# Performance work log

Measured on AMD Instinct MI355X. Metric: run time of the kernel, lower is better.

Reference implementation:

```python
import jax, jax.numpy as jnp
import numpy as np

B, S, D = 1024, 200, 128
NQ, NC, NQD, NCD = 50000, 1000, 101, 101


def _linear_params(k, fan_in, fan_out):
    bound = 1.0 / np.sqrt(fan_in)
    kw, kb = jax.random.split(k)
    W = jax.random.uniform(kw, (fan_out, fan_in), minval=-bound, maxval=bound, dtype=jnp.float32)
    b = jax.random.uniform(kb, (fan_out,), minval=-bound, maxval=bound, dtype=jnp.float32)
    return W, b


def setup_inputs() -> dict:
    key = jax.random.key(0)
    ks = jax.random.split(key, 17)
    Wx, bx = _linear_params(ks[0], 4 * D, D)
    Ws1, bs1 = _linear_params(ks[1], D, D)
    Ws2, bs2 = _linear_params(ks[2], D, D)
    Wp1, bp1 = _linear_params(ks[3], 2 * D, D)
    Wp2, bp2 = _linear_params(ks[4], 2 * D, D)
    Wk, bk = _linear_params(ks[5], 4 * D, D)
    Eq = jax.random.normal(ks[6], (NQ, D), dtype=jnp.float32)
    Ec = jax.random.normal(ks[7], (NC, D), dtype=jnp.float32)
    Eqd = jax.random.normal(ks[8], (NQD, D), dtype=jnp.float32)
    Ecd = jax.random.normal(ks[9], (NCD, D), dtype=jnp.float32)
    Ecorr = jax.random.normal(ks[10], (2, D), dtype=jnp.float32)
    # xavier_uniform init for h_pre (torch: gain*sqrt(6/(fan_in+fan_out)) on [B,D])
    bh = np.sqrt(6.0 / (B + D))
    h0 = jax.random.uniform(ks[11], (B, D), minval=-bh, maxval=bh, dtype=jnp.float32)
    question_seq = jax.random.randint(ks[12], (B, S), 0, NQ)
    concept_seq = jax.random.randint(ks[13], (B, S), 0, NC)
    question_diff_seq = jax.random.randint(ks[14], (B, S), 0, NQD)
    concept_diff_seq = jax.random.randint(ks[15], (B, S), 0, NCD)
    correct_seq = jax.random.randint(ks[16], (B, S), 0, 2)
    return dict(question_seq=question_seq, concept_seq=concept_seq,
                question_diff_seq=question_diff_seq, concept_diff_seq=concept_diff_seq,
                correct_seq=correct_seq,
                Eq=Eq, Ec=Ec, Eqd=Eqd, Ecd=Ecd, Ecorr=Ecorr,
                Wx=Wx, bx=bx, Ws1=Ws1, bs1=bs1, Ws2=Ws2, bs2=bs2,
                Wp1=Wp1, bp1=bp1, Wp2=Wp2, bp2=bp2, Wk=Wk, bk=bk, h0=h0)


def reference(question_seq, concept_seq, question_diff_seq, concept_diff_seq, correct_seq,
              Eq, Ec, Eqd, Ecd, Ecorr,
              Wx, bx, Ws1, bs1, Ws2, bs2, Wp1, bp1, Wp2, bp2, Wk, bk, h0):
    qe = Eq[question_seq]            # [B,S,D]
    ce = Ec[concept_seq]
    qde = Eqd[question_diff_seq]
    cde = Ecd[concept_diff_seq]
    corr = Ecorr[correct_seq]
    # generate_x_MLP applied to all timesteps at once (same math as per-step)
    x = jnp.concatenate([qe, ce, qde, cde], axis=-1) @ Wx.T + bx  # [B,S,D]
    # time-major inputs for the scan over t = 0 .. S-2
    xs = (jnp.swapaxes(x[:, :-1], 0, 1),      # x_t       [S-1,B,D]
          jnp.swapaxes(x[:, 1:], 0, 1),       # x_{t+1}
          jnp.swapaxes(corr[:, :-1], 0, 1),
          jnp.swapaxes(qde[:, :-1], 0, 1),
          jnp.swapaxes(cde[:, :-1], 0, 1))

    def step(h_pre, inp):
        xt, xnext, ct, qdt, cdt = inp
        s_in = xt - h_pre
        sdf = jax.nn.sigmoid(s_in @ Ws1.T + bs1) * jnp.tanh(s_in @ Ws2.T + bs2)  # dropout=eval identity
        p_in = jnp.concatenate([sdf, ct], axis=-1)
        pka = jax.nn.sigmoid(p_in @ Wp1.T + bp1) * jnp.tanh(p_in @ Wp2.T + bp2)
        k_in = jnp.concatenate([h_pre, ct, qdt, cdt], axis=-1)
        g = jax.nn.sigmoid(k_in @ Wk.T + bk)
        h = g * h_pre + (1.0 - g) * pka
        yt = jax.nn.sigmoid(jnp.sum(xnext * h, axis=-1))  # [B]
        return h, yt

    _, ys = jax.lax.scan(step, h0, xs)  # ys: [S-1,B]
    y = jnp.concatenate([ys.T, jnp.zeros((question_seq.shape[0], 1), x.dtype)], axis=1)  # [B,S], y[:, S-1]=0
    return y
```

## Files before the change

kernel.cpp:

```cpp
#include <hip/hip_runtime.h>
#include <hip/hip_bf16.h>


#define S_LEN 200
#define NBATCH 1024
#define DIM 128
#define LOG2E 1.4426950408889634f

typedef short short8 __attribute__((ext_vector_type(8)));
typedef float f32x4 __attribute__((ext_vector_type(4)));

__device__ __forceinline__ unsigned short f2b(float f) {
  union { float f; unsigned u; } v; v.f = f;
  unsigned r = (v.u + 0x7FFFu + ((v.u >> 16) & 1u)) >> 16;
  return (unsigned short)r;
}
__device__ __forceinline__ float b2f(unsigned short b) {
  union { unsigned u; float f; } v; v.u = ((unsigned)b) << 16;
  return v.f;
}
__device__ __forceinline__ unsigned pk_bf16(float lo, float hi) {
  __hip_bfloat162 t = __float22bfloat162_rn(make_float2(lo, hi));
  union { __hip_bfloat162 h; unsigned u; } cv; cv.h = t;
  return cv.u;
}
__device__ __forceinline__ float sigtanh(float a, float b) {
  a = fminf(a, 30.0f);
  b = fminf(b, 15.0f);
  const float u = __builtin_amdgcn_exp2f(LOG2E * a);
  const float v = __builtin_amdgcn_exp2f(2.0f * LOG2E * b);
  return (u * (v - 1.0f)) * __builtin_amdgcn_rcpf((1.0f + u) * (v + 1.0f));
}
__device__ __forceinline__ float fast_sigmoid(float x) {
  x = fmaxf(x, -30.0f);
  return __builtin_amdgcn_rcpf(1.0f + __builtin_amdgcn_exp2f(-LOG2E * x));
}
__device__ __forceinline__ void wg_barrier_lds() {
  __asm__ volatile("s_waitcnt lgkmcnt(0)\n\ts_barrier" ::: "memory");
}

__global__ void proj_all_kernel(const float* __restrict__ Eq, const float* __restrict__ Ec,
                                const float* __restrict__ Eqd, const float* __restrict__ Ecd,
                                const float* __restrict__ Ecorr,
                                const float* __restrict__ Wx,
                                const float* __restrict__ Wp1, const float* __restrict__ bp1,
                                const float* __restrict__ Wp2, const float* __restrict__ bp2,
                                const float* __restrict__ Wk, const float* __restrict__ bk,
                                unsigned short* __restrict__ Tq, unsigned short* __restrict__ Tc,
                                unsigned short* __restrict__ Tqd, unsigned short* __restrict__ Tcd,
                                unsigned short* __restrict__ Tkqd, unsigned short* __restrict__ Tkcd,
                                float* __restrict__ Tkc, float* __restrict__ Tp1c,
                                float* __restrict__ Tp2c) {
  const int bid = blockIdx.x;
  const int tid = threadIdx.x;
  if (bid >= 802) {
    const int blk = bid - 802;
    if (blk < 101) {
      const int o = tid & 127, half = tid >> 7;
      const float* e = (half ? Ecd : Eqd) + (size_t)blk * DIM;
      const float* wr = Wk + (size_t)o * 512 + (half ? 384 : 256);
      float a = 0.f;
      for (int k = 0; k < DIM; ++k) a = fmaf(e[k], wr[k], a);
      (half ? Tkcd : Tkqd)[blk * DIM + o] = f2b(a);
    } else {
      for (int idx = tid; idx < 768; idx += 256) {
        const int t = idx >> 8, e = (idx >> 7) & 1, o = idx & 127;
        const float* ec = Ecorr + e * DIM;
        const float* wr; float bias; float* dst;
        if (t == 0)      { wr = Wp1 + (size_t)o * 256 + 128; bias = bp1[o]; dst = Tp1c; }
        else if (t == 1) { wr = Wp2 + (size_t)o * 256 + 128; bias = bp2[o]; dst = Tp2c; }
        else             { wr = Wk  + (size_t)o * 512 + 128; bias = bk[o];  dst = Tkc;  }
        float a = bias;
        for (int k = 0; k < DIM; ++k) a = fmaf(ec[k], wr[k], a);
        dst[e * DIM + o] = a;
      }
    }
    return;
  }
  const float* E; int M, coff, r0; unsigned short* T;
  if (bid < 782)      { E = Eq;  M = 50000; coff = 0;   T = Tq;  r0 = bid * 64; }
  else if (bid < 798) { E = Ec;  M = 1000;  coff = 128; T = Tc;  r0 = (bid - 782) * 64; }
  else if (bid < 800) { E = Eqd; M = 101;   coff = 256; T = Tqd; r0 = (bid - 798) * 64; }
  else                { E = Ecd; M = 101;   coff = 384; T = Tcd; r0 = (bid - 800) * 64; }

  __shared__ __align__(16) unsigned short A[64][136];
  {
    const int row = tid >> 2, cb = (tid & 3) * 32;
    union U8 { uint4 v; unsigned short s[8]; } o;
#pragma unroll
    for (int cc = 0; cc < 4; ++cc) {
      const int c8 = cb + cc * 8;
      if (r0 + row < M) {
        const float4 e0 = *(const float4*)(E + (size_t)(r0 + row) * DIM + c8);
        const float4 e1 = *(const float4*)(E + (size_t)(r0 + row) * DIM + c8 + 4);
        o.s[0] = f2b(e0.x); o.s[1] = f2b(e0.y); o.s[2] = f2b(e0.z); o.s[3] = f2b(e0.w);
        o.s[4] = f2b(e1.x); o.s[5] = f2b(e1.y); o.s[6] = f2b(e1.z); o.s[7] = f2b(e1.w);
      } else {
        o.v = make_uint4(0, 0, 0, 0);
      }
      *(uint4*)&A[row][c8] = o.v;
    }
  }
  __syncthreads();
  const int w = tid >> 6, L = tid & 63, q = L >> 4, m = L & 15;
  short8 bf[2][4];
#pragma unroll
  for (int T2 = 0; T2 < 2; ++T2) {
    const int n = 32 * w + 16 * T2 + m;
#pragma unroll
    for (int kb = 0; kb < 4; ++kb) {
      const float* src = Wx + (size_t)n * 512 + coff + kb * 32 + q * 8;
      const float4 v0 = *(const float4*)src;
      const float4 v1 = *(const float4*)(src + 4);
      short8 f;
      f[0] = (short)f2b(v0.x); f[1] = (short)f2b(v0.y);
      f[2] = (short)f2b(v0.z); f[3] = (short)f2b(v0.w);
      f[4] = (short)f2b(v1.x); f[5] = (short)f2b(v1.y);
      f[6] = (short)f2b(v1.z); f[7] = (short)f2b(v1.w);
      bf[T2][kb] = f;
    }
  }
  const f32x4 vzero = {0.f, 0.f, 0.f, 0.f};
#pragma unroll
  for (int mt = 0; mt < 4; ++mt) {
    short8 af[4];
#pragma unroll
    for (int kb = 0; kb < 4; ++kb) af[kb] = *(const short8*)&A[mt * 16 + m][kb * 32 + q * 8];
    f32x4 acc[2] = {vzero, vzero};
#pragma unroll
    for (int kb = 0; kb < 4; ++kb) {
#pragma unroll
      for (int T2 = 0; T2 < 2; ++T2)
        acc[T2] = __builtin_amdgcn_mfma_f32_16x16x32_bf16(af[kb], bf[T2][kb], acc[T2], 0, 0, 0);
    }
#pragma unroll
    for (int T2 = 0; T2 < 2; ++T2) {
      const int col = 32 * w + 16 * T2 + m;
#pragma unroll
      for (int i = 0; i < 4; ++i) {
        const int r = r0 + mt * 16 + q * 4 + i;
        if (r < M) T[(size_t)r * DIM + col] = f2b(acc[T2][i]);
      }
    }
  }
}

__global__ void build_x_kernel(const int* __restrict__ qs, const int* __restrict__ cs,
                               const int* __restrict__ qds, const int* __restrict__ cds,
                               const int* __restrict__ corr,
                               const unsigned short* __restrict__ Tq, const unsigned short* __restrict__ Tc,
                               const unsigned short* __restrict__ Tqd, const unsigned short* __restrict__ Tcd,
                               const float* __restrict__ bx, unsigned short* __restrict__ xg,
                               float* __restrict__ corrf) {
  const int r0 = blockIdx.x * 32;
  const int c8 = (threadIdx.x & 15) * 8;
  const float4 bx0 = *(const float4*)(bx + c8);
  const float4 bx1 = *(const float4*)(bx + c8 + 4);
  float bb[8] = {bx0.x, bx0.y, bx0.z, bx0.w, bx1.x, bx1.y, bx1.z, bx1.w};
  union U8 { uint4 v; unsigned short s[8]; };
#pragma unroll
  for (int half = 0; half < 2; ++half) {
    const int r = r0 + (threadIdx.x >> 4) + half * 16;
    const int s = r >> 10, b = r & 1023;
    const int q = qs[b * S_LEN + s], c = cs[b * S_LEN + s];
    const int qd = qds[b * S_LEN + s], cd = cds[b * S_LEN + s];
    U8 vq, vc, vd, ve, o;
    vq.v = *(const uint4*)(Tq + (size_t)q * DIM + c8);
    vc.v = *(const uint4*)(Tc + (size_t)c * DIM + c8);
    vd.v = *(const uint4*)(Tqd + (size_t)qd * DIM + c8);
    ve.v = *(const uint4*)(Tcd + (size_t)cd * DIM + c8);
#pragma unroll
    for (int j = 0; j < 8; ++j)
      o.s[j] = f2b(b2f(vq.s[j]) + b2f(vc.s[j]) + b2f(vd.s[j]) + b2f(ve.s[j]) + bb[j]);
    *(uint4*)(xg + (size_t)r * DIM + c8) = o.v;
    if ((threadIdx.x & 15) == 0) corrf[r] = (float)corr[b * S_LEN + s];
  }
}

__global__ void gemm_xg_kernel(const unsigned short* __restrict__ xg,
                               const float* __restrict__ Wk,
                               const int* __restrict__ corr, const int* __restrict__ qds,
                               const int* __restrict__ cds,
                               const float* __restrict__ Tkc,
                               const unsigned short* __restrict__ Tkqd,
                               const unsigned short* __restrict__ Tkcd,
                               unsigned short* __restrict__ GG) {
  const int tid = threadIdx.x;
  const int r0 = blockIdx.x * 128;
  __shared__ __align__(16) unsigned short TS[128][136];
#pragma unroll
  for (int it = 0; it < 2; ++it) {
    const int idx = tid + 256 * it;
    const int row = idx >> 2, cb = (idx & 3) * 32;
    const int r = r0 + row, t = r >> 10, b = r & 1023;
    const int ci = corr[b * S_LEN + t], qi = qds[b * S_LEN + t], di = cds[b * S_LEN + t];
    union U8 { uint4 v; unsigned short s[8]; };
#pragma unroll
    for (int cc = 0; cc < 4; ++cc) {
      const int c8 = cb + cc * 8;
      U8 vq, vc, o;
      vq.v = *(const uint4*)(Tkqd + (size_t)qi * DIM + c8);
      vc.v = *(const uint4*)(Tkcd + (size_t)di * DIM + c8);
      const float4 k0 = *(const float4*)(Tkc + (size_t)ci * DIM + c8);
      const float4 k1 = *(const float4*)(Tkc + (size_t)ci * DIM + c8 + 4);
      float kk[8] = {k0.x, k0.y, k0.z, k0.w, k1.x, k1.y, k1.z, k1.w};
#pragma unroll
      for (int j = 0; j < 8; ++j) o.s[j] = f2b(kk[j] + b2f(vq.s[j]) + b2f(vc.s[j]));
      *(uint4*)&TS[row][c8] = o.v;
    }
  }
  __syncthreads();
  const int w = tid >> 6, L = tid & 63, q = L >> 4, m = L & 15;
  short8 wk[2][4];
#pragma unroll
  for (int T = 0; T < 2; ++T) {
    const int n = 32 * w + 16 * T + m;
#pragma unroll
    for (int kb = 0; kb < 4; ++kb) {
      const float* src = Wk + (size_t)n * 512 + kb * 32 + q * 8;
      const float4 v0 = *(const float4*)src;
      const float4 v1 = *(const float4*)(src + 4);
      short8 f;
      f[0] = (short)f2b(v0.x); f[1] = (short)f2b(v0.y);
      f[2] = (short)f2b(v0.z); f[3] = (short)f2b(v0.w);
      f[4] = (short)f2b(v1.x); f[5] = (short)f2b(v1.y);
      f[6] = (short)f2b(v1.z); f[7] = (short)f2b(v1.w);
      wk[T][kb] = f;
    }
  }
  const f32x4 vzero = {0.f, 0.f, 0.f, 0.f};
#pragma unroll
  for (int mt = 0; mt < 8; ++mt) {
    short8 af[4];
#pragma unroll
    for (int kb = 0; kb < 4; ++kb)
      af[kb] = *(const short8*)(xg + (size_t)(r0 + mt * 16 + m) * DIM + kb * 32 + q * 8);
    f32x4 acc[2] = {vzero, vzero};
#pragma unroll
    for (int kb = 0; kb < 4; ++kb) {
#pragma unroll
      for (int T = 0; T < 2; ++T)
        acc[T] = __builtin_amdgcn_mfma_f32_16x16x32_bf16(af[kb], wk[T][kb], acc[T], 0, 0, 0);
    }
#pragma unroll
    for (int T = 0; T < 2; ++T) {
      const int col = 32 * w + 16 * T + m;
#pragma unroll
      for (int i = 0; i < 4; ++i) {
        const int row128 = mt * 16 + q * 4 + i;
        GG[(size_t)(r0 + row128) * DIM + col] = f2b(acc[T][i] + b2f(TS[row128][col]));
      }
    }
  }
}

__global__ __launch_bounds__(512, 2) void scan_kernel(
    const unsigned short* __restrict__ xg,
    const unsigned short* __restrict__ gg,
    const float* __restrict__ corrf,
    const float* __restrict__ h0,
    const float* __restrict__ Ws1, const float* __restrict__ bs1,
    const float* __restrict__ Ws2, const float* __restrict__ bs2,
    const float* __restrict__ Wp1, const float* __restrict__ Wp2,
    const float* __restrict__ Wk,
    const float* __restrict__ gTp1c, const float* __restrict__ gTp2c,
    float* __restrict__ outp) {
  __shared__ __align__(16) unsigned short Sbuf[16][136];
  __shared__ __align__(16) unsigned short Pbuf[16][136];
  __shared__ float DotBuf[16][9];

  const int tid = threadIdx.x;
  const int w = tid >> 6, L = tid & 63, q = L >> 4, m = L & 15;
  const int col16 = 16 * w + m;
  const int rbase = blockIdx.x << 4;
  const size_t SB = (size_t)NBATCH * DIM;

  short8 wf[5][4];
  {
    const float* Wptr[5] = {Ws1, Ws2, Wp1, Wp2, Wk};
    const int ldw[5] = {128, 128, 256, 256, 512};
#pragma unroll
    for (int M = 0; M < 5; ++M) {
#pragma unroll
      for (int kb = 0; kb < 4; ++kb) {
        const float* src = Wptr[M] + (size_t)col16 * ldw[M] + kb * 32 + q * 8;
        const float4 v0 = *(const float4*)src;
        const float4 v1 = *(const float4*)(src + 4);
        short8 f;
        f[0] = (short)f2b(v0.x); f[1] = (short)f2b(v0.y);
        f[2] = (short)f2b(v0.z); f[3] = (short)f2b(v0.w);
        f[4] = (short)f2b(v1.x); f[5] = (short)f2b(v1.y);
        f[6] = (short)f2b(v1.z); f[7] = (short)f2b(v1.w);
        wf[M][kb] = f;
      }
    }
  }
  const float bs1v = bs1[col16], bs2v = bs2[col16];
  const float tp1v0 = gTp1c[col16], dtp1 = gTp1c[DIM + col16] - tp1v0;
  const float tp2v0 = gTp2c[col16], dtp2 = gTp2c[DIM + col16] - tp2v0;

  float h[4];
#pragma unroll
  for (int i = 0; i < 4; ++i) {
    const int b = rbase + q * 4 + i;
    const float hv = h0[(size_t)b * DIM + col16];
    h[i] = hv;
    const float xt = b2f(xg[(size_t)b * DIM + col16]);
    Sbuf[q * 4 + i][col16] = f2b(xt - hv);
  }
  if (tid < 16) outp[(size_t)(rbase + tid) * S_LEN + (S_LEN - 1)] = 0.0f;

  unsigned short XPA[4], XPB[4], GPA[4], GPB[4];
  float4 CFA, CFB;
  const unsigned short* pxA = xg + 3 * SB + (size_t)(rbase + q * 4) * DIM + col16;
  const unsigned short* pxB = pxA + SB;
  const unsigned short* pgA = gg + 2 * SB + (size_t)(rbase + q * 4) * DIM + col16;
  const unsigned short* pgB = pgA + SB;
  const float* pcA = corrf + 2 * NBATCH + rbase + q * 4;
  const float* pcB = pcA + NBATCH;
#pragma unroll
  for (int i = 0; i < 4; ++i) {
    XPA[i] = xg[SB + (size_t)(rbase + q * 4 + i) * DIM + col16];
    XPB[i] = xg[2 * SB + (size_t)(rbase + q * 4 + i) * DIM + col16];
    GPA[i] = gg[(size_t)(rbase + q * 4 + i) * DIM + col16];
    GPB[i] = gg[SB + (size_t)(rbase + q * 4 + i) * DIM + col16];
  }
  CFA = *(const float4*)(corrf + rbase + q * 4);
  CFB = *(const float4*)(corrf + NBATCH + rbase + q * 4);

  float dotp[4] = {0.f, 0.f, 0.f, 0.f};
  const f32x4 vzero = {0.f, 0.f, 0.f, 0.f};

#define STEP(TCUR, XP, GP, CF, PX, PG, PC)                                     \
  do {                                                                         \
    const int t_ = (TCUR);                                                     \
    wg_barrier_lds();                  \
      \
    short8 sf[4];                                                              \
    _Pragma("unroll") for (int kb = 0; kb < 4; ++kb)                           \
        sf[kb] = *(const short8*)&Sbuf[m][kb * 32 + q * 8];                    \
    float xnv[4], ggv[4], cfv[4];                                              \
    _Pragma("unroll") for (int i = 0; i < 4; ++i) {                            \
      xnv[i] = b2f(XP[i]); ggv[i] = b2f(GP[i]);                                \
    }                                                                          \
    cfv[0] = CF.x; cfv[1] = CF.y; cfv[2] = CF.z; cfv[3] = CF.w;                \
    _Pragma("unroll") for (int i = 0; i < 4; ++i) {                            \
      XP[i] = PX[i * DIM]; GP[i] = PG[i * DIM];                                \
    }                                                                          \
    CF = *(const float4*)PC;                                                   \
    PX += 2 * SB; PG += 2 * SB; PC += 2 * NBATCH;                              \
    {                  \
      float dr0 = dotp[0], dr1 = dotp[1], dr2 = dotp[2], dr3 = dotp[3];        \
      _Pragma("unroll") for (int off = 1; off <= 8; off <<= 1) {               \
        dr0 += __shfl_xor(dr0, off, 64);                                       \
        dr1 += __shfl_xor(dr1, off, 64);                                       \
        dr2 += __shfl_xor(dr2, off, 64);                                       \
        dr3 += __shfl_xor(dr3, off, 64);                                       \
      }                                                                        \
      if (m == 0) {                                                            \
        DotBuf[q * 4 + 0][w] = dr0;                                            \
        DotBuf[q * 4 + 1][w] = dr1;                                            \
        DotBuf[q * 4 + 2][w] = dr2;                                            \
        DotBuf[q * 4 + 3][w] = dr3;                                            \
      }                                                                        \
    }                                                                          \
    f32x4 a1 = vzero, a2 = vzero, c1 = vzero;                                  \
    _Pragma("unroll") for (int kb = 0; kb < 4; ++kb) {                         \
      a1 = __builtin_amdgcn_mfma_f32_16x16x32_bf16(sf[kb], wf[0][kb], a1, 0, 0, 0); \
      a2 = __builtin_amdgcn_mfma_f32_16x16x32_bf16(sf[kb], wf[1][kb], a2, 0, 0, 0); \
      c1 = __builtin_amdgcn_mfma_f32_16x16x32_bf16(sf[kb], wf[4][kb], c1, 0, 0, 0); \
    }                                                                          \
    _Pragma("unroll") for (int i2 = 0; i2 < 2; ++i2) {                         \
      const float s0 = sigtanh(a1[2 * i2] + bs1v, a2[2 * i2] + bs2v);          \
      const float s1 = sigtanh(a1[2 * i2 + 1] + bs1v, a2[2 * i2 + 1] + bs2v);  \
      const unsigned u = pk_bf16(s0, s1);                                      \
      Pbuf[q * 4 + 2 * i2][col16] = (unsigned short)u;                         \
      Pbuf[q * 4 + 2 * i2 + 1][col16] = (unsigned short)(u >> 16);             \
    }                                                                          \
    wg_barrier_lds();                                 \
    short8 pf[4];                                                              \
    _Pragma("unroll") for (int kb = 0; kb < 4; ++kb)                           \
        pf[kb] = *(const short8*)&Pbuf[m][kb * 32 + q * 8];                    \
    if (t_ > 0 && tid < 16) {          \
      float d = 0.f;                                                           \
      _Pragma("unroll") for (int ww = 0; ww < 8; ++ww) d += DotBuf[tid][ww];   \
      outp[(size_t)(rbase + tid) * S_LEN + (t_ - 1)] = fast_sigmoid(d);        \
    }                                                                          \
    f32x4 p1 = vzero, p2 = vzero;                                              \
    _Pragma("unroll") for (int kb = 0; kb < 4; ++kb) {                         \
      p1 = __builtin_amdgcn_mfma_f32_16x16x32_bf16(pf[kb], wf[2][kb], p1, 0, 0, 0); \
      p2 = __builtin_amdgcn_mfma_f32_16x16x32_bf16(pf[kb], wf[3][kb], p2, 0, 0, 0); \
    }                                                                          \
    float sn[4];                                                               \
    _Pragma("unroll") for (int i = 0; i < 4; ++i) {                            \
      const float g = fast_sigmoid(ggv[i] - c1[i]);                            \
      const float t1v = fmaf(cfv[i], dtp1, tp1v0);                             \
      const float t2v = fmaf(cfv[i], dtp2, tp2v0);                             \
      const float pka = sigtanh(p1[i] + t1v, p2[i] + t2v);                     \
      const float hn = pka + g * (h[i] - pka);                                 \
      h[i] = hn;                                                               \
      sn[i] = xnv[i] - hn;                                                     \
      dotp[i] = xnv[i] * hn;                                                   \
    }                                                                          \
    _Pragma("unroll") for (int i2 = 0; i2 < 2; ++i2) {                         \
      const unsigned u = pk_bf16(sn[2 * i2], sn[2 * i2 + 1]);                  \
      Sbuf[q * 4 + 2 * i2][col16] = (unsigned short)u;                         \
      Sbuf[q * 4 + 2 * i2 + 1][col16] = (unsigned short)(u >> 16);             \
    }                                                                          \
  } while (0)

  for (int t2 = 0; t2 < 198; t2 += 2) {
    STEP(t2, XPA, GPA, CFA, pxA, pgA, pcA);
    STEP(t2 + 1, XPB, GPB, CFB, pxB, pgB, pcB);
  }
  STEP(198, XPA, GPA, CFA, pxA, pgA, pcA);
#undef STEP

  {
    float dr0 = dotp[0], dr1 = dotp[1], dr2 = dotp[2], dr3 = dotp[3];
#pragma unroll
    for (int off = 1; off <= 8; off <<= 1) {
      dr0 += __shfl_xor(dr0, off, 64);
      dr1 += __shfl_xor(dr1, off, 64);
      dr2 += __shfl_xor(dr2, off, 64);
      dr3 += __shfl_xor(dr3, off, 64);
    }
    if (m == 0) {
      DotBuf[q * 4 + 0][w] = dr0;
      DotBuf[q * 4 + 1][w] = dr1;
      DotBuf[q * 4 + 2][w] = dr2;
      DotBuf[q * 4 + 3][w] = dr3;
    }
  }
  wg_barrier_lds();
  if (tid < 16) {
    float d = 0.f;
#pragma unroll
    for (int ww = 0; ww < 8; ++ww) d += DotBuf[tid][ww];
    outp[(size_t)(rbase + tid) * S_LEN + (S_LEN - 2)] = fast_sigmoid(d);
  }
}

extern "C" void kernel_launch(void* const* d_in, const int* in_sizes, int n_in,
                              void* d_out, int out_size, void* d_ws, size_t ws_size,
                              hipStream_t stream) {
  const int* qs    = (const int*)d_in[0];
  const int* cs    = (const int*)d_in[1];
  const int* qds   = (const int*)d_in[2];
  const int* cds   = (const int*)d_in[3];
  const int* corr  = (const int*)d_in[4];
  const float* Eq    = (const float*)d_in[5];
  const float* Ec    = (const float*)d_in[6];
  const float* Eqd   = (const float*)d_in[7];
  const float* Ecd   = (const float*)d_in[8];
  const float* Ecorr = (const float*)d_in[9];
  const float* Wx  = (const float*)d_in[10];
  const float* bx  = (const float*)d_in[11];
  const float* Ws1 = (const float*)d_in[12];
  const float* bs1 = (const float*)d_in[13];
  const float* Ws2 = (const float*)d_in[14];
  const float* bs2 = (const float*)d_in[15];
  const float* Wp1 = (const float*)d_in[16];
  const float* bp1 = (const float*)d_in[17];
  const float* Wp2 = (const float*)d_in[18];
  const float* bp2 = (const float*)d_in[19];
  const float* Wk  = (const float*)d_in[20];
  const float* bk  = (const float*)d_in[21];
  const float* h0  = (const float*)d_in[22];

  char* ws = (char*)d_ws;
  const size_t xbytes = (size_t)S_LEN * NBATCH * DIM * 2;
  const size_t A = (xbytes + 255) & ~(size_t)255;
  const size_t ggbytes = (size_t)(S_LEN - 1) * NBATCH * DIM * 2;
  unsigned short* X  = (unsigned short*)ws;
  unsigned short* GG = (unsigned short*)(ws + A);
  unsigned short* Tq  = GG;
  unsigned short* Tc  = (unsigned short*)(ws + A + (size_t)50000 * DIM * 2);
  unsigned short* Tqd = (unsigned short*)(ws + A + (size_t)51000 * DIM * 2);
  unsigned short* Tcd = (unsigned short*)(ws + A + (size_t)51101 * DIM * 2);
  size_t off = A + ((ggbytes + 255) & ~(size_t)255);
  auto alloc = [&](size_t bytes) {
    void* p = ws + off;
    off = (off + bytes + 255) & ~(size_t)255;
    return p;
  };
  float* corrf = (float*)alloc((size_t)S_LEN * NBATCH * 4);
  unsigned short* Tkqd = (unsigned short*)alloc((size_t)101 * DIM * 2);
  unsigned short* Tkcd = (unsigned short*)alloc((size_t)101 * DIM * 2);
  float* Tkc  = (float*)alloc((size_t)2 * DIM * 4);
  float* Tp1c = (float*)alloc((size_t)2 * DIM * 4);
  float* Tp2c = (float*)alloc((size_t)2 * DIM * 4);

  proj_all_kernel<<<904, 256, 0, stream>>>(Eq, Ec, Eqd, Ecd, Ecorr, Wx,
                                           Wp1, bp1, Wp2, bp2, Wk, bk,
                                           Tq, Tc, Tqd, Tcd, Tkqd, Tkcd, Tkc, Tp1c, Tp2c);
  build_x_kernel<<<(S_LEN * NBATCH) / 32, 256, 0, stream>>>(qs, cs, qds, cds, corr,
                                                            Tq, Tc, Tqd, Tcd, bx, X, corrf);
  gemm_xg_kernel<<<((S_LEN - 1) * NBATCH) / 128, 256, 0, stream>>>(X, Wk, corr, qds, cds,
                                                                   Tkc, Tkqd, Tkcd, GG);
  scan_kernel<<<64, 512, 0, stream>>>(X, GG, corrf, h0, Ws1, bs1, Ws2, bs2,
                                      Wp1, Wp2, Wk, Tp1c, Tp2c, (float*)d_out);
}
```

Baseline: 546.9 us.

## Double scan block to 1024 threads, split rows across wave halves, stage Wp weights in LDS

The scan kernel now runs 16 waves per block instead of 8. Each pair of waves computes the same 16-column MFMA tiles redundantly but handles only two of the four output rows in the pointwise epilogue, which halves the per-thread sigmoid/tanh work. To free registers, the Wp1/Wp2 bf16 fragments are moved from VGPRs into LDS and reloaded every step, and the loop is no longer unrolled by two. The gain in per-wave latency comes at the cost of duplicated MFMA work, barriers across twice as many waves, and extra LDS reads on the serial critical path.

```diff
diff --git a/kernel.cpp b/kernel.cpp
--- a/kernel.cpp
+++ b/kernel.cpp
@@ -254,7 +254,8 @@
   }
 }
 
-__global__ __launch_bounds__(512, 2) void scan_kernel(
+#define SEL(V, i) (hb ? (V)[2 + (i)] : (V)[(i)])
+__global__ __launch_bounds__(1024, 4) void scan_kernel(
     const unsigned short* __restrict__ xg,
     const unsigned short* __restrict__ gg,
     const float* __restrict__ corrf,
@@ -267,20 +268,46 @@
     float* __restrict__ outp) {
   __shared__ __align__(16) unsigned short Sbuf[16][136];
   __shared__ __align__(16) unsigned short Pbuf[16][136];
+  __shared__ __align__(16) unsigned short Wp1L[128][136];
+  __shared__ __align__(16) unsigned short Wp2L[128][136];
   __shared__ float DotBuf[16][9];
 
   const int tid = threadIdx.x;
-  const int w = tid >> 6, L = tid & 63, q = L >> 4, m = L & 15;
-  const int col16 = 16 * w + m;
+  const int w16 = tid >> 6;
+  const int wc = w16 & 7;
+  const int hb = (w16 >> 3) << 1;
+  const int L = tid & 63, q = L >> 4, m = L & 15;
+  const int col16 = 16 * wc + m;
   const int rbase = blockIdx.x << 4;
   const size_t SB = (size_t)NBATCH * DIM;
 
-  short8 wf[5][4];
   {
-    const float* Wptr[5] = {Ws1, Ws2, Wp1, Wp2, Wk};
-    const int ldw[5] = {128, 128, 256, 256, 512};
-#pragma unroll
-    for (int M = 0; M < 5; ++M) {
+    const int n = tid >> 3;
+    const int c0 = (tid & 7) * 16;
+    const float* s1 = Wp1 + (size_t)n * 256 + c0;
+    const float* s2 = Wp2 + (size_t)n * 256 + c0;
+    union U8 { uint4 v; unsigned short s[8]; } o;
+#pragma unroll
+    for (int hh = 0; hh < 2; ++hh) {
+      float4 a = *(const float4*)(s1 + hh * 8);
+      float4 b = *(const float4*)(s1 + hh * 8 + 4);
+      o.s[0] = f2b(a.x); o.s[1] = f2b(a.y); o.s[2] = f2b(a.z); o.s[3] = f2b(a.w);
+      o.s[4] = f2b(b.x); o.s[5] = f2b(b.y); o.s[6] = f2b(b.z); o.s[7] = f2b(b.w);
+      *(uint4*)&Wp1L[n][c0 + hh * 8] = o.v;
+      a = *(const float4*)(s2 + hh * 8);
+      b = *(const float4*)(s2 + hh * 8 + 4);
+      o.s[0] = f2b(a.x); o.s[1] = f2b(a.y); o.s[2] = f2b(a.z); o.s[3] = f2b(a.w);
+      o.s[4] = f2b(b.x); o.s[5] = f2b(b.y); o.s[6] = f2b(b.z); o.s[7] = f2b(b.w);
+      *(uint4*)&Wp2L[n][c0 + hh * 8] = o.v;
+    }
+  }
+
+  short8 wf[3][4];
+  {
+    const float* Wptr[3] = {Ws1, Ws2, Wk};
+    const int ldw[3] = {128, 128, 512};
+#pragma unroll
+    for (int M = 0; M < 3; ++M) {
 #pragma unroll
       for (int kb = 0; kb < 4; ++kb) {
         const float* src = Wptr[M] + (size_t)col16 * ldw[M] + kb * 32 + q * 8;
@@ -299,137 +326,122 @@
   const float tp1v0 = gTp1c[col16], dtp1 = gTp1c[DIM + col16] - tp1v0;
   const float tp2v0 = gTp2c[col16], dtp2 = gTp2c[DIM + col16] - tp2v0;
 
-  float h[4];
-#pragma unroll
-  for (int i = 0; i < 4; ++i) {
-    const int b = rbase + q * 4 + i;
+  float h[2];
+#pragma unroll
+  for (int i = 0; i < 2; ++i) {
+    const int row = q * 4 + hb + i;
+    const int b = rbase + row;
     const float hv = h0[(size_t)b * DIM + col16];
     h[i] = hv;
     const float xt = b2f(xg[(size_t)b * DIM + col16]);
-    Sbuf[q * 4 + i][col16] = f2b(xt - hv);
+    Sbuf[row][col16] = f2b(xt - hv);
   }
   if (tid < 16) outp[(size_t)(rbase + tid) * S_LEN + (S_LEN - 1)] = 0.0f;
 
-  unsigned short XPA[4], XPB[4], GPA[4], GPB[4];
-  float4 CFA, CFB;
-  const unsigned short* pxA = xg + 3 * SB + (size_t)(rbase + q * 4) * DIM + col16;
-  const unsigned short* pxB = pxA + SB;
-  const unsigned short* pgA = gg + 2 * SB + (size_t)(rbase + q * 4) * DIM + col16;
-  const unsigned short* pgB = pgA + SB;
-  const float* pcA = corrf + 2 * NBATCH + rbase + q * 4;
-  const float* pcB = pcA + NBATCH;
-#pragma unroll
-  for (int i = 0; i < 4; ++i) {
-    XPA[i] = xg[SB + (size_t)(rbase + q * 4 + i) * DIM + col16];
-    XPB[i] = xg[2 * SB + (size_t)(rbase + q * 4 + i) * DIM + col16];
-    GPA[i] = gg[(size_t)(rbase + q * 4 + i) * DIM + col16];
-    GPB[i] = gg[SB + (size_t)(rbase + q * 4 + i) * DIM + col16];
-  }
-  CFA = *(const float4*)(corrf + rbase + q * 4);
-  CFB = *(const float4*)(corrf + NBATCH + rbase + q * 4);
-
-  float dotp[4] = {0.f, 0.f, 0.f, 0.f};
+  unsigned short XP[2], GP[2];
+  float2 CF;
+  const unsigned short* px = xg + 2 * SB + (size_t)(rbase + q * 4 + hb) * DIM + col16;
+  const unsigned short* pg = gg + 1 * SB + (size_t)(rbase + q * 4 + hb) * DIM + col16;
+  const float* pc = corrf + 1 * NBATCH + rbase + q * 4 + hb;
+#pragma unroll
+  for (int i = 0; i < 2; ++i) {
+    XP[i] = xg[SB + (size_t)(rbase + q * 4 + hb + i) * DIM + col16];
+    GP[i] = gg[(size_t)(rbase + q * 4 + hb + i) * DIM + col16];
+  }
+  CF = *(const float2*)(corrf + rbase + q * 4 + hb);
+
+  float dotp[2] = {0.f, 0.f};
   const f32x4 vzero = {0.f, 0.f, 0.f, 0.f};
 
-#define STEP(TCUR, XP, GP, CF, PX, PG, PC)                                     \
-  do {                                                                         \
-    const int t_ = (TCUR);                                                     \
-    wg_barrier_lds();                  \
-      \
-    short8 sf[4];                                                              \
-    _Pragma("unroll") for (int kb = 0; kb < 4; ++kb)                           \
-        sf[kb] = *(const short8*)&Sbuf[m][kb * 32 + q * 8];                    \
-    float xnv[4], ggv[4], cfv[4];                                              \
-    _Pragma("unroll") for (int i = 0; i < 4; ++i) {                            \
-      xnv[i] = b2f(XP[i]); ggv[i] = b2f(GP[i]);                                \
-    }                                                                          \
-    cfv[0] = CF.x; cfv[1] = CF.y; cfv[2] = CF.z; cfv[3] = CF.w;                \
-    _Pragma("unroll") for (int i = 0; i < 4; ++i) {                            \
-      XP[i] = PX[i * DIM]; GP[i] = PG[i * DIM];                                \
-    }                                                                          \
-    CF = *(const float4*)PC;                                                   \
-    PX += 2 * SB; PG += 2 * SB; PC += 2 * NBATCH;                              \
-    {                  \
-      float dr0 = dotp[0], dr1 = dotp[1], dr2 = dotp[2], dr3 = dotp[3];        \
-      _Pragma("unroll") for (int off = 1; off <= 8; off <<= 1) {               \
-        dr0 += __shfl_xor(dr0, off, 64);                                       \
-        dr1 += __shfl_xor(dr1, off, 64);                                       \
-        dr2 += __shfl_xor(dr2, off, 64);                                       \
-        dr3 += __shfl_xor(dr3, off, 64);                                       \
-      }                                                                        \
-      if (m == 0) {                                                            \
-        DotBuf[q * 4 + 0][w] = dr0;                                            \
-        DotBuf[q * 4 + 1][w] = dr1;                                            \
-        DotBuf[q * 4 + 2][w] = dr2;                                            \
-        DotBuf[q * 4 + 3][w] = dr3;                                            \
-      }                                                                        \
-    }                                                                          \
-    f32x4 a1 = vzero, a2 = vzero, c1 = vzero;                                  \
-    _Pragma("unroll") for (int kb = 0; kb < 4; ++kb) {                         \
-      a1 = __builtin_amdgcn_mfma_f32_16x16x32_bf16(sf[kb], wf[0][kb], a1, 0, 0, 0); \
-      a2 = __builtin_amdgcn_mfma_f32_16x16x32_bf16(sf[kb], wf[1][kb], a2, 0, 0, 0); \
-      c1 = __builtin_amdgcn_mfma_f32_16x16x32_bf16(sf[kb], wf[4][kb], c1, 0, 0, 0); \
-    }                                                                          \
-    _Pragma("unroll") for (int i2 = 0; i2 < 2; ++i2) {                         \
-      const float s0 = sigtanh(a1[2 * i2] + bs1v, a2[2 * i2] + bs2v);          \
-      const float s1 = sigtanh(a1[2 * i2 + 1] + bs1v, a2[2 * i2 + 1] + bs2v);  \
-      const unsigned u = pk_bf16(s0, s1);                                      \
-      Pbuf[q * 4 + 2 * i2][col16] = (unsigned short)u;                         \
-      Pbuf[q * 4 + 2 * i2 + 1][col16] = (unsigned short)(u >> 16);             \
-    }                                                                          \
-    wg_barrier_lds();                                 \
-    short8 pf[4];                                                              \
-    _Pragma("unroll") for (int kb = 0; kb < 4; ++kb)                           \
-        pf[kb] = *(const short8*)&Pbuf[m][kb * 32 + q * 8];                    \
-    if (t_ > 0 && tid < 16) {          \
-      float d = 0.f;                                                           \
-      _Pragma("unroll") for (int ww = 0; ww < 8; ++ww) d += DotBuf[tid][ww];   \
-      outp[(size_t)(rbase + tid) * S_LEN + (t_ - 1)] = fast_sigmoid(d);        \
-    }                                                                          \
-    f32x4 p1 = vzero, p2 = vzero;                                              \
-    _Pragma("unroll") for (int kb = 0; kb < 4; ++kb) {                         \
-      p1 = __builtin_amdgcn_mfma_f32_16x16x32_bf16(pf[kb], wf[2][kb], p1, 0, 0, 0); \
-      p2 = __builtin_amdgcn_mfma_f32_16x16x32_bf16(pf[kb], wf[3][kb], p2, 0, 0, 0); \
-    }                                                                          \
-    float sn[4];                                                               \
-    _Pragma("unroll") for (int i = 0; i < 4; ++i) {                            \
-      const float g = fast_sigmoid(ggv[i] - c1[i]);                            \
-      const float t1v = fmaf(cfv[i], dtp1, tp1v0);                             \
-      const float t2v = fmaf(cfv[i], dtp2, tp2v0);                             \
-      const float pka = sigtanh(p1[i] + t1v, p2[i] + t2v);                     \
-      const float hn = pka + g * (h[i] - pka);                                 \
-      h[i] = hn;                                                               \
-      sn[i] = xnv[i] - hn;                                                     \
-      dotp[i] = xnv[i] * hn;                                                   \
-    }                                                                          \
-    _Pragma("unroll") for (int i2 = 0; i2 < 2; ++i2) {                         \
-      const unsigned u = pk_bf16(sn[2 * i2], sn[2 * i2 + 1]);                  \
-      Sbuf[q * 4 + 2 * i2][col16] = (unsigned short)u;                         \
-      Sbuf[q * 4 + 2 * i2 + 1][col16] = (unsigned short)(u >> 16);             \
-    }                                                                          \
-  } while (0)
-
-  for (int t2 = 0; t2 < 198; t2 += 2) {
-    STEP(t2, XPA, GPA, CFA, pxA, pgA, pcA);
-    STEP(t2 + 1, XPB, GPB, CFB, pxB, pgB, pcB);
-  }
-  STEP(198, XPA, GPA, CFA, pxA, pgA, pcA);
-#undef STEP
+#pragma unroll 1
+  for (int t = 0; t < S_LEN - 1; ++t) {
+    float xnv[2] = {b2f(XP[0]), b2f(XP[1])};
+    float ggv[2] = {b2f(GP[0]), b2f(GP[1])};
+    const float cf0 = CF.x, cf1 = CF.y;
+    XP[0] = px[0]; XP[1] = px[DIM];
+    GP[0] = pg[0]; GP[1] = pg[DIM];
+    CF = *(const float2*)pc;
+    px += SB; pg += SB; pc += NBATCH;
+
+    wg_barrier_lds();
+    short8 sf[4];
+#pragma unroll
+    for (int kb = 0; kb < 4; ++kb) sf[kb] = *(const short8*)&Sbuf[m][kb * 32 + q * 8];
+    {
+      float d0 = dotp[0], d1 = dotp[1];
+#pragma unroll
+      for (int off = 1; off <= 8; off <<= 1) {
+        d0 += __shfl_xor(d0, off, 64);
+        d1 += __shfl_xor(d1, off, 64);
+      }
+      if (m == 0) {
+        DotBuf[q * 4 + hb + 0][wc] = d0;
+        DotBuf[q * 4 + hb + 1][wc] = d1;
+      }
+    }
+    f32x4 a1 = vzero, a2 = vzero, c1 = vzero;
+#pragma unroll
+    for (int kb = 0; kb < 4; ++kb) {
+      a1 = __builtin_amdgcn_mfma_f32_16x16x32_bf16(sf[kb], wf[0][kb], a1, 0, 0, 0);
+      a2 = __builtin_amdgcn_mfma_f32_16x16x32_bf16(sf[kb], wf[1][kb], a2, 0, 0, 0);
+      c1 = __builtin_amdgcn_mfma_f32_16x16x32_bf16(sf[kb], wf[2][kb], c1, 0, 0, 0);
+    }
+    {
+      const float s0 = sigtanh(SEL(a1, 0) + bs1v, SEL(a2, 0) + bs2v);
+      const float s1 = sigtanh(SEL(a1, 1) + bs1v, SEL(a2, 1) + bs2v);
+      const unsigned u = pk_bf16(s0, s1);
+      Pbuf[q * 4 + hb + 0][col16] = (unsigned short)u;
+      Pbuf[q * 4 + hb + 1][col16] = (unsigned short)(u >> 16);
+    }
+    wg_barrier_lds();
+    short8 pf[4];
+#pragma unroll
+    for (int kb = 0; kb < 4; ++kb) pf[kb] = *(const short8*)&Pbuf[m][kb * 32 + q * 8];
+    if (t > 0 && tid < 16) {
+      float d = 0.f;
+#pragma unroll
+      for (int ww = 0; ww < 8; ++ww) d += DotBuf[tid][ww];
+      outp[(size_t)(rbase + tid) * S_LEN + (t - 1)] = fast_sigmoid(d);
+    }
+    f32x4 p1 = vzero, p2 = vzero;
+#pragma unroll
+    for (int kb = 0; kb < 4; ++kb) {
+      const short8 w1 = *(const short8*)&Wp1L[col16][kb * 32 + q * 8];
+      p1 = __builtin_amdgcn_mfma_f32_16x16x32_bf16(pf[kb], w1, p1, 0, 0, 0);
+      const short8 w2 = *(const short8*)&Wp2L[col16][kb * 32 + q * 8];
+      p2 = __builtin_amdgcn_mfma_f32_16x16x32_bf16(pf[kb], w2, p2, 0, 0, 0);
+    }
+    float sn[2];
+    {
+      const float g0 = fast_sigmoid(ggv[0] - SEL(c1, 0));
+      const float g1 = fast_sigmoid(ggv[1] - SEL(c1, 1));
+      const float pka0 = sigtanh(SEL(p1, 0) + fmaf(cf0, dtp1, tp1v0),
+                                 SEL(p2, 0) + fmaf(cf0, dtp2, tp2v0));
+      const float pka1 = sigtanh(SEL(p1, 1) + fmaf(cf1, dtp1, tp1v0),
+                                 SEL(p2, 1) + fmaf(cf1, dtp2, tp2v0));
+      const float hn0 = pka0 + g0 * (h[0] - pka0);
+      const float hn1 = pka1 + g1 * (h[1] - pka1);
+      h[0] = hn0; h[1] = hn1;
+      sn[0] = xnv[0] - hn0; sn[1] = xnv[1] - hn1;
+      dotp[0] = xnv[0] * hn0; dotp[1] = xnv[1] * hn1;
+    }
+    {
+      const unsigned u = pk_bf16(sn[0], sn[1]);
+      Sbuf[q * 4 + hb + 0][col16] = (unsigned short)u;
+      Sbuf[q * 4 + hb + 1][col16] = (unsigned short)(u >> 16);
+    }
+  }
 
   {
-    float dr0 = dotp[0], dr1 = dotp[1], dr2 = dotp[2], dr3 = dotp[3];
+    float d0 = dotp[0], d1 = dotp[1];
 #pragma unroll
     for (int off = 1; off <= 8; off <<= 1) {
-      dr0 += __shfl_xor(dr0, off, 64);
-      dr1 += __shfl_xor(dr1, off, 64);
-      dr2 += __shfl_xor(dr2, off, 64);
-      dr3 += __shfl_xor(dr3, off, 64);
+      d0 += __shfl_xor(d0, off, 64);
+      d1 += __shfl_xor(d1, off, 64);
     }
     if (m == 0) {
-      DotBuf[q * 4 + 0][w] = dr0;
-      DotBuf[q * 4 + 1][w] = dr1;
-      DotBuf[q * 4 + 2][w] = dr2;
-      DotBuf[q * 4 + 3][w] = dr3;
+      DotBuf[q * 4 + hb + 0][wc] = d0;
+      DotBuf[q * 4 + hb + 1][wc] = d1;
     }
   }
   wg_barrier_lds();
@@ -498,6 +510,6 @@
                                                             Tq, Tc, Tqd, Tcd, bx, X, corrf);
   gemm_xg_kernel<<<((S_LEN - 1) * NBATCH) / 128, 256, 0, stream>>>(X, Wk, corr, qds, cds,
                                                                    Tkc, Tkqd, Tkcd, GG);
-  scan_kernel<<<64, 512, 0, stream>>>(X, GG, corrf, h0, Ws1, bs1, Ws2, bs2,
-                                      Wp1, Wp2, Wk, Tp1c, Tp2c, (float*)d_out);
-}
+  scan_kernel<<<64, 1024, 0, stream>>>(X, GG, corrf, h0, Ws1, bs1, Ws2, bs2,
+                                       Wp1, Wp2, Wk, Tp1c, Tp2c, (float*)d_out);
+}
```

Result: slower. 657.3 us (+20.2%).
